# Performance work log

Hardware: AMD Instinct MI355X
Metric: run time of the kernel (lower is better)

Reference implementation:

```python
import jax, jax.numpy as jnp
import numpy as np

EPS = 1e-5  # torch LayerNorm default

def _ln(x, g, b):
    m = jnp.mean(x, axis=-1, keepdims=True)
    v = jnp.mean((x - m) ** 2, axis=-1, keepdims=True)
    return (x - m) * jax.lax.rsqrt(v + EPS) * g + b

def setup_inputs() -> dict:
    key = jax.random.key(0)
    ks = jax.random.split(key, 12)
    N_sup = N_res = 768
    c_z = 128   # input_dim
    c = 128     # num_intermediate_channel
    c_out = 128 # output_dim
    s = 0.02
    d = {}
    d["act_s"] = jax.random.normal(ks[0], (N_sup, N_sup, c_z), jnp.float32)
    d["act_r"] = jax.random.normal(ks[1], (N_res, N_res, c_z), jnp.float32)
    d["mask_r"] = (jax.random.uniform(ks[2], (N_res, N_res)) > 0.1).astype(jnp.float32)
    # input LayerNorm params
    d["ln_in_g"] = jnp.ones((c_z,), jnp.float32)
    d["ln_in_b"] = jnp.zeros((c_z,), jnp.float32)
    # projections (stored as [in, out], y = x @ W + b)
    d["w_lp"] = (jax.random.normal(ks[3], (c_z, c)) * s).astype(jnp.float32)
    d["b_lp"] = jnp.zeros((c,), jnp.float32)
    d["w_rp"] = (jax.random.normal(ks[4], (c_z, c)) * s).astype(jnp.float32)
    d["b_rp"] = jnp.zeros((c,), jnp.float32)
    # gates (bias_init=1)
    d["w_lg"] = (jax.random.normal(ks[5], (c_z, c)) * s).astype(jnp.float32)
    d["b_lg"] = jnp.ones((c,), jnp.float32)
    d["w_rg"] = (jax.random.normal(ks[6], (c_z, c)) * s).astype(jnp.float32)
    d["b_rg"] = jnp.ones((c,), jnp.float32)
    # center LayerNorm
    d["ln_c_g"] = jnp.ones((c,), jnp.float32)
    d["ln_c_b"] = jnp.zeros((c,), jnp.float32)
    # output projection
    d["w_out"] = (jax.random.normal(ks[7], (c, c_out)) * s).astype(jnp.float32)
    d["b_out"] = jnp.zeros((c_out,), jnp.float32)
    return d

def reference(act_s, act_r, mask_r, ln_in_g, ln_in_b, w_lp, b_lp, w_rp, b_rp,
              w_lg, b_lg, w_rg, b_rg, ln_c_g, ln_c_b, w_out, b_out):
    m = mask_r[..., None]                                   # [N_res, N_res, 1]
    s = _ln(act_s, ln_in_g, ln_in_b)                        # [N_sup, N_sup, c_z]
    r = _ln(act_r, ln_in_g, ln_in_b)                        # [N_res, N_res, c_z]
    left = (s @ w_lp + b_lp) * jax.nn.sigmoid(s @ w_lg + b_lg)
    right = (m * (r @ w_rp + b_rp)) * jax.nn.sigmoid(r @ w_rg + b_rg)
    left_line = left.sum(axis=0)                            # [N_sup, c] (aggr_by_row)
    right_line = right.sum(axis=0)                          # [N_res, c]
    act = jnp.einsum('ik,jk->ijk', left_line, right_line)   # [N_sup, N_res, c]
    act = _ln(act, ln_c_g, ln_c_b)
    return act @ w_out + b_out                              # [N_sup, N_res, c_out]
```

## Files before the change

### kernel.cpp

```cpp
#include <hip/hip_runtime.h>
#include <math.h>

#define NRES 768
#define C    128
#define LNEPS 1e-5f
#define TA   16
#define ACH  48
#define MI   16
#define NIT  (NRES / MI)
#define XBUF (MI * 256)

typedef __attribute__((ext_vector_type(8))) short bf16x8;
typedef __attribute__((ext_vector_type(4))) float f32x4;

__device__ __forceinline__ uint32_t bf16rn(float f) {
    uint32_t u = __float_as_uint(f);
    return (u + 0x7FFFu + ((u >> 16) & 1u)) >> 16;
}

__device__ __forceinline__ void split2(float a, float b, uint32_t& hi, uint32_t& lo) {
    uint32_t ha = bf16rn(a), hb = bf16rn(b);
    float ra = a - __uint_as_float(ha << 16);
    float rb = b - __uint_as_float(hb << 16);
    hi = ha | (hb << 16);
    lo = bf16rn(ra) | (bf16rn(rb) << 16);
}

__device__ __forceinline__ void stage_row3(const float4& x, int row, int t,
                                           char* hiB, char* loB, char* sqB) {
    const int byte = (row * 256 + 8 * (t & 31)) ^ ((row & 15) << 4);
    uint2 uh, ul, uq;
    split2(x.x, x.y, uh.x, ul.x);
    split2(x.z, x.w, uh.y, ul.y);
    uq.x = bf16rn(x.x * x.x) | (bf16rn(x.y * x.y) << 16);
    uq.y = bf16rn(x.z * x.z) | (bf16rn(x.w * x.w) << 16);
    *(uint2*)(hiB + byte) = uh;
    *(uint2*)(loB + byte) = ul;
    *(uint2*)(sqB + byte) = uq;
}

template <int RIGHT>
__global__ __launch_bounds__(256, 3) void line_mfma(
    const float* __restrict__ act,
    const float* __restrict__ mask,
    const float* __restrict__ ln_g, const float* __restrict__ ln_b,
    const float* __restrict__ wP, const float* __restrict__ bP,
    const float* __restrict__ wG, const float* __restrict__ bG,
    float* __restrict__ part)
{
    __shared__ char  sHi[XBUF];
    __shared__ char  sLo[XBUF];
    __shared__ char  sSq[XBUF];
    __shared__ float sM[TA * MI];

    const int t = threadIdx.x;
    const int w = t >> 6;
    const int l = t & 63;
    const int i0  = (blockIdx.x % NIT) * MI;
    const int ach = blockIdx.x / NIT;
    const int a0  = ach * TA;

    bf16x8 bfr[4][4];
    float  sQ[4], cB[4];
#pragma unroll
    for (int nt = 0; nt < 4; ++nt) {
        const float* wsrc = (nt < 2) ? wP : wG;
        const int n = w * 32 + (nt & 1) * 16 + (l & 15);
        float sacc = 0.f, tacc = 0.f;
#pragma unroll
        for (int kk = 0; kk < 4; ++kk) {
            bf16x8 f;
#pragma unroll
            for (int jj = 0; jj < 8; ++jj) {
                const int k = kk * 32 + (l >> 4) * 8 + jj;
                const float wv = wsrc[k * C + n];
                const uint32_t q = bf16rn(ln_g[k] * wv);
                f[jj] = (short)q;
                sacc += __uint_as_float(q << 16);
                tacc += ln_b[k] * wv;
            }
            bfr[nt][kk] = f;
        }
        sacc += __shfl_xor(sacc, 16); sacc += __shfl_xor(sacc, 32);
        tacc += __shfl_xor(tacc, 16); tacc += __shfl_xor(tacc, 32);
        sQ[nt] = sacc;
        cB[nt] = tacc + ((nt < 2) ? bP[n] : bG[n]);
    }

    bf16x8 onesf;
#pragma unroll
    for (int jj = 0; jj < 8; ++jj) onesf[jj] = (short)0x3F80;

    if (RIGHT) {
        sM[t] = mask[(size_t)(a0 + (t >> 4)) * NRES + i0 + (t & 15)];
    }

    float lacc[2][4];
#pragma unroll
    for (int ntp = 0; ntp < 2; ++ntp)
#pragma unroll
        for (int jr = 0; jr < 4; ++jr) lacc[ntp][jr] = 0.f;

    const float* srcbase = act + (size_t)a0 * (NRES * C) + (size_t)i0 * C;

    float4 xv[2], xn[2];
#pragma unroll
    for (int j = 0; j < 2; ++j)
        xv[j] = *(const float4*)(srcbase + 4 * (t + 256 * j));

    for (int al = 0; al < TA; ++al) {
        if (al + 1 < TA) {
            const float* srcn = srcbase + (size_t)(al + 1) * (NRES * C);
#pragma unroll
            for (int j = 0; j < 2; ++j)
                xn[j] = *(const float4*)(srcn + 4 * (t + 256 * j));
        }

#pragma unroll
        for (int j = 0; j < 2; ++j)
            stage_row3(xv[j], (t >> 5) + 8 * j, t, sHi, sLo, sSq);
        __syncthreads();

        const f32x4 zero = {0.f, 0.f, 0.f, 0.f};
        f32x4 acc[4], accS = zero, accS2 = zero;
#pragma unroll
        for (int nt = 0; nt < 4; ++nt) acc[nt] = zero;

#pragma unroll
        for (int kk = 0; kk < 4; ++kk) {
            const int row  = l & 15;
            const int byte = (row * 256 + (kk * 32 + (l >> 4) * 8) * 2) ^ ((row & 15) << 4);
            const bf16x8 ah  = *(const bf16x8*)(sHi + byte);
            const bf16x8 alo = *(const bf16x8*)(sLo + byte);
            const bf16x8 asq = *(const bf16x8*)(sSq + byte);
            acc[0] = __builtin_amdgcn_mfma_f32_16x16x32_bf16(ah,  bfr[0][kk], acc[0], 0, 0, 0);
            acc[0] = __builtin_amdgcn_mfma_f32_16x16x32_bf16(alo, bfr[0][kk], acc[0], 0, 0, 0);
            acc[1] = __builtin_amdgcn_mfma_f32_16x16x32_bf16(ah,  bfr[1][kk], acc[1], 0, 0, 0);
            acc[1] = __builtin_amdgcn_mfma_f32_16x16x32_bf16(alo, bfr[1][kk], acc[1], 0, 0, 0);
            acc[2] = __builtin_amdgcn_mfma_f32_16x16x32_bf16(ah,  bfr[2][kk], acc[2], 0, 0, 0);
            acc[3] = __builtin_amdgcn_mfma_f32_16x16x32_bf16(ah,  bfr[3][kk], acc[3], 0, 0, 0);
            accS  = __builtin_amdgcn_mfma_f32_16x16x32_bf16(ah,  onesf, accS,  0, 0, 0);
            accS2 = __builtin_amdgcn_mfma_f32_16x16x32_bf16(asq, onesf, accS2, 0, 0, 0);
        }

        float mk[4] = {1.f, 1.f, 1.f, 1.f};
        if (RIGHT) {
            const float4 m4 = *(const float4*)&sM[al * MI + (l >> 4) * 4];
            mk[0] = m4.x; mk[1] = m4.y; mk[2] = m4.z; mk[3] = m4.w;
        }
#pragma unroll
        for (int jr = 0; jr < 4; ++jr) {
            const float m_  = accS[jr] * (1.f / C);
            const float var = accS2[jr] * (1.f / C) - m_ * m_;
            const float inv = rsqrtf(var + LNEPS);
#pragma unroll
            for (int ntp = 0; ntp < 2; ++ntp) {
                const float P = (acc[ntp][jr]     - m_ * sQ[ntp])     * inv + cB[ntp];
                const float G = (acc[ntp + 2][jr] - m_ * sQ[ntp + 2]) * inv + cB[ntp + 2];
                const float sg = __builtin_amdgcn_rcpf(1.f + __expf(-G));
                lacc[ntp][jr] += P * sg * mk[jr];
            }
        }
        __syncthreads();

        xv[0] = xn[0]; xv[1] = xn[1];
    }

    float* dst = part + (size_t)ach * (NRES * C);
#pragma unroll
    for (int ntp = 0; ntp < 2; ++ntp)
#pragma unroll
        for (int jr = 0; jr < 4; ++jr)
            dst[(size_t)(i0 + (l >> 4) * 4 + jr) * C +
                w * 32 + ntp * 16 + (l & 15)] = lacc[ntp][jr];
}

__global__ __launch_bounds__(256) void reduce_part(const float* __restrict__ part,
                                                   float* __restrict__ line) {
    const int idx = blockIdx.x * 256 + threadIdx.x;
    float s = 0.f;
#pragma unroll 8
    for (int p = 0; p < ACH; ++p) s += part[(size_t)p * (NRES * C) + idx];
    line[idx] = s;
}

__global__ __launch_bounds__(256, 3) void out_mfma(
    const float* __restrict__ lline,
    const float* __restrict__ rline,
    const float* __restrict__ cg, const float* __restrict__ cb,
    const float* __restrict__ wO, const float* __restrict__ bO,
    float* __restrict__ out)
{
    __shared__ char sHi[64 * 256];
    __shared__ char sLo[64 * 256];
    __shared__ char sSq[64 * 256];

    const int t = threadIdx.x;
    const int w = t >> 6;
    const int l = t & 63;
    const int i  = blockIdx.x / 12;
    const int j0 = (blockIdx.x % 12) * 64;

    bf16x8 bfr[2][4];
    float  sQ[2], cB[2];
#pragma unroll
    for (int nt = 0; nt < 2; ++nt) {
        const int n = w * 32 + nt * 16 + (l & 15);
        float sacc = 0.f, tacc = 0.f;
#pragma unroll
        for (int kk = 0; kk < 4; ++kk) {
            bf16x8 f;
#pragma unroll
            for (int jj = 0; jj < 8; ++jj) {
                const int k = kk * 32 + (l >> 4) * 8 + jj;
                const float wv = wO[k * C + n];
                const uint32_t q = bf16rn(cg[k] * wv);
                f[jj] = (short)q;
                sacc += __uint_as_float(q << 16);
                tacc += cb[k] * wv;
            }
            bfr[nt][kk] = f;
        }
        sacc += __shfl_xor(sacc, 16); sacc += __shfl_xor(sacc, 32);
        tacc += __shfl_xor(tacc, 16); tacc += __shfl_xor(tacc, 32);
        sQ[nt] = sacc;
        cB[nt] = tacc + bO[n];
    }

    bf16x8 onesf;
#pragma unroll
    for (int jj = 0; jj < 8; ++jj) onesf[jj] = (short)0x3F80;

    const int c4 = 4 * (t & 31);
    const float4 l4 = *(const float4*)(lline + (size_t)i * C + c4);

    const float* rsrc = rline + (size_t)j0 * C;
#pragma unroll
    for (int j = 0; j < 8; ++j) {
        const float4 r = *(const float4*)(rsrc + 4 * (t + 256 * j));
        float4 p;
        p.x = l4.x * r.x; p.y = l4.y * r.y; p.z = l4.z * r.z; p.w = l4.w * r.w;
        stage_row3(p, (t >> 5) + 8 * j, t, sHi, sLo, sSq);
    }
    __syncthreads();

    const f32x4 zero = {0.f, 0.f, 0.f, 0.f};
#pragma unroll
    for (int mt = 0; mt < 4; ++mt) {
        f32x4 acc[2], accS = zero, accS2 = zero;
#pragma unroll
        for (int nt = 0; nt < 2; ++nt) acc[nt] = zero;
#pragma unroll
        for (int kk = 0; kk < 4; ++kk) {
            const int row  = mt * 16 + (l & 15);
            const int byte = (row * 256 + (kk * 32 + (l >> 4) * 8) * 2) ^ ((row & 15) << 4);
            const bf16x8 ah  = *(const bf16x8*)(sHi + byte);
            const bf16x8 alo = *(const bf16x8*)(sLo + byte);
            const bf16x8 asq = *(const bf16x8*)(sSq + byte);
            acc[0] = __builtin_amdgcn_mfma_f32_16x16x32_bf16(ah,  bfr[0][kk], acc[0], 0, 0, 0);
            acc[0] = __builtin_amdgcn_mfma_f32_16x16x32_bf16(alo, bfr[0][kk], acc[0], 0, 0, 0);
            acc[1] = __builtin_amdgcn_mfma_f32_16x16x32_bf16(ah,  bfr[1][kk], acc[1], 0, 0, 0);
            acc[1] = __builtin_amdgcn_mfma_f32_16x16x32_bf16(alo, bfr[1][kk], acc[1], 0, 0, 0);
            accS  = __builtin_amdgcn_mfma_f32_16x16x32_bf16(ah,  onesf, accS,  0, 0, 0);
            accS2 = __builtin_amdgcn_mfma_f32_16x16x32_bf16(asq, onesf, accS2, 0, 0, 0);
        }
#pragma unroll
        for (int jr = 0; jr < 4; ++jr) {
            const float m_  = accS[jr] * (1.f / C);
            const float var = accS2[jr] * (1.f / C) - m_ * m_;
            const float inv = rsqrtf(var + LNEPS);
#pragma unroll
            for (int nt = 0; nt < 2; ++nt)
                out[((size_t)i * NRES + j0 + mt * 16 + (l >> 4) * 4 + jr) * C +
                    w * 32 + nt * 16 + (l & 15)] =
                    (acc[nt][jr] - m_ * sQ[nt]) * inv + cB[nt];
        }
    }
}

extern "C" void kernel_launch(void* const* d_in, const int* in_sizes, int n_in,
                              void* d_out, int out_size, void* d_ws, size_t ws_size,
                              hipStream_t stream) {
    const float* act_s = (const float*)d_in[0];
    const float* act_r = (const float*)d_in[1];
    const float* mask  = (const float*)d_in[2];
    const float* ln_g  = (const float*)d_in[3];
    const float* ln_b  = (const float*)d_in[4];
    const float* w_lp  = (const float*)d_in[5];
    const float* b_lp  = (const float*)d_in[6];
    const float* w_rp  = (const float*)d_in[7];
    const float* b_rp  = (const float*)d_in[8];
    const float* w_lg  = (const float*)d_in[9];
    const float* b_lg  = (const float*)d_in[10];
    const float* w_rg  = (const float*)d_in[11];
    const float* b_rg  = (const float*)d_in[12];
    const float* ln_cg = (const float*)d_in[13];
    const float* ln_cb = (const float*)d_in[14];
    const float* w_out = (const float*)d_in[15];
    const float* b_out = (const float*)d_in[16];
    float* out = (float*)d_out;

    float* part       = (float*)d_ws;
    float* left_line  = part + (size_t)ACH * NRES * C;
    float* right_line = left_line + NRES * C;

    line_mfma<0><<<ACH * NIT, 256, 0, stream>>>(act_s, nullptr, ln_g, ln_b,
                                                w_lp, b_lp, w_lg, b_lg, part);
    reduce_part<<<NRES * C / 256, 256, 0, stream>>>(part, left_line);
    line_mfma<1><<<ACH * NIT, 256, 0, stream>>>(act_r, mask, ln_g, ln_b,
                                                w_rp, b_rp, w_rg, b_rg, part);
    reduce_part<<<NRES * C / 256, 256, 0, stream>>>(part, right_line);
    out_mfma<<<NRES * 12, 256, 0, stream>>>(left_line, right_line, ln_cg, ln_cb,
                                            w_out, b_out, out);
}
```

Baseline: 366.4 us.

## Merge left/right line kernels, fuse reductions, loop output tiles per block

Merges the left and right line-projection kernels into one launch and the two reductions into one, which removes launches and lets both halves share the GPU at once. The out kernel now gives each block a whole output row and loops over 12 column tiles, so the weight fragments are built once per row instead of once per tile. The staging split switches from round-to-nearest to truncation for the hi/lo/square bf16 parts, which is cheaper but can change numerics slightly. The risks are a larger partial-sum workspace and only 768 output blocks with a serial tile loop, which may cut parallelism and latency hiding.

Result: faster. 337.3 us (-8.0%).

```diff
diff --git a/kernel.cpp b/kernel.cpp
--- a/kernel.cpp
+++ b/kernel.cpp
@@ -9,43 +9,49 @@
 #define MI   16
 #define NIT  (NRES / MI)
 #define XBUF (MI * 256)
+#define LHALF (ACH * NIT)
 
 typedef __attribute__((ext_vector_type(8))) short bf16x8;
 typedef __attribute__((ext_vector_type(4))) float f32x4;
 
-__device__ __forceinline__ uint32_t bf16rn(float f) {
-    uint32_t u = __float_as_uint(f);
-    return (u + 0x7FFFu + ((u >> 16) & 1u)) >> 16;
-}
-
-__device__ __forceinline__ void split2(float a, float b, uint32_t& hi, uint32_t& lo) {
-    uint32_t ha = bf16rn(a), hb = bf16rn(b);
-    float ra = a - __uint_as_float(ha << 16);
-    float rb = b - __uint_as_float(hb << 16);
-    hi = ha | (hb << 16);
-    lo = bf16rn(ra) | (bf16rn(rb) << 16);
+__device__ __forceinline__ uint32_t pack_hi(uint32_t u0, uint32_t u1) {
+    return (u1 & 0xFFFF0000u) | (u0 >> 16);
+}
+
+__device__ __forceinline__ void split2t(float a, float b, uint32_t& hi, uint32_t& lo) {
+    const uint32_t ua = __float_as_uint(a), ub = __float_as_uint(b);
+    const float ra = a - __uint_as_float(ua & 0xFFFF0000u);
+    const float rb = b - __uint_as_float(ub & 0xFFFF0000u);
+    hi = pack_hi(ua, ub);
+    lo = pack_hi(__float_as_uint(ra), __float_as_uint(rb));
 }
 
 __device__ __forceinline__ void stage_row3(const float4& x, int row, int t,
                                            char* hiB, char* loB, char* sqB) {
     const int byte = (row * 256 + 8 * (t & 31)) ^ ((row & 15) << 4);
     uint2 uh, ul, uq;
-    split2(x.x, x.y, uh.x, ul.x);
-    split2(x.z, x.w, uh.y, ul.y);
-    uq.x = bf16rn(x.x * x.x) | (bf16rn(x.y * x.y) << 16);
-    uq.y = bf16rn(x.z * x.z) | (bf16rn(x.w * x.w) << 16);
+    split2t(x.x, x.y, uh.x, ul.x);
+    split2t(x.z, x.w, uh.y, ul.y);
+    uq.x = pack_hi(__float_as_uint(x.x * x.x), __float_as_uint(x.y * x.y));
+    uq.y = pack_hi(__float_as_uint(x.z * x.z), __float_as_uint(x.w * x.w));
     *(uint2*)(hiB + byte) = uh;
     *(uint2*)(loB + byte) = ul;
     *(uint2*)(sqB + byte) = uq;
 }
 
-template <int RIGHT>
-__global__ __launch_bounds__(256, 3) void line_mfma(
-    const float* __restrict__ act,
+__device__ __forceinline__ uint32_t bf16rn(float f) {
+    uint32_t u = __float_as_uint(f);
+    return (u + 0x7FFFu + ((u >> 16) & 1u)) >> 16;
+}
+
+__global__ __launch_bounds__(256, 3) void line_all(
+    const float* __restrict__ act_s, const float* __restrict__ act_r,
     const float* __restrict__ mask,
     const float* __restrict__ ln_g, const float* __restrict__ ln_b,
-    const float* __restrict__ wP, const float* __restrict__ bP,
-    const float* __restrict__ wG, const float* __restrict__ bG,
+    const float* __restrict__ w_lp, const float* __restrict__ b_lp,
+    const float* __restrict__ w_rp, const float* __restrict__ b_rp,
+    const float* __restrict__ w_lg, const float* __restrict__ b_lg,
+    const float* __restrict__ w_rg, const float* __restrict__ b_rg,
     float* __restrict__ part)
 {
     __shared__ char  sHi[XBUF];
@@ -56,9 +62,17 @@
     const int t = threadIdx.x;
     const int w = t >> 6;
     const int l = t & 63;
-    const int i0  = (blockIdx.x % NIT) * MI;
-    const int ach = blockIdx.x / NIT;
+    const int right = (blockIdx.x >= LHALF);
+    const int bid2  = blockIdx.x - right * LHALF;
+    const int i0  = (bid2 % NIT) * MI;
+    const int ach = bid2 / NIT;
     const int a0  = ach * TA;
+
+    const float* act = right ? act_r : act_s;
+    const float* wP  = right ? w_rp : w_lp;
+    const float* bP  = right ? b_rp : b_lp;
+    const float* wG  = right ? w_rg : w_lg;
+    const float* bG  = right ? b_rg : b_lg;
 
     bf16x8 bfr[4][4];
     float  sQ[4], cB[4];
@@ -91,7 +105,7 @@
 #pragma unroll
     for (int jj = 0; jj < 8; ++jj) onesf[jj] = (short)0x3F80;
 
-    if (RIGHT) {
+    if (right) {
         sM[t] = mask[(size_t)(a0 + (t >> 4)) * NRES + i0 + (t & 15)];
     }
 
@@ -139,12 +153,12 @@
             acc[1] = __builtin_amdgcn_mfma_f32_16x16x32_bf16(alo, bfr[1][kk], acc[1], 0, 0, 0);
             acc[2] = __builtin_amdgcn_mfma_f32_16x16x32_bf16(ah,  bfr[2][kk], acc[2], 0, 0, 0);
             acc[3] = __builtin_amdgcn_mfma_f32_16x16x32_bf16(ah,  bfr[3][kk], acc[3], 0, 0, 0);
-            accS  = __builtin_amdgcn_mfma_f32_16x16x32_bf16(ah,  onesf, accS,  0, 0, 0);
-            accS2 = __builtin_amdgcn_mfma_f32_16x16x32_bf16(asq, onesf, accS2, 0, 0, 0);
+            accS   = __builtin_amdgcn_mfma_f32_16x16x32_bf16(ah,  onesf, accS,  0, 0, 0);
+            accS2  = __builtin_amdgcn_mfma_f32_16x16x32_bf16(asq, onesf, accS2, 0, 0, 0);
         }
 
         float mk[4] = {1.f, 1.f, 1.f, 1.f};
-        if (RIGHT) {
+        if (right) {
             const float4 m4 = *(const float4*)&sM[al * MI + (l >> 4) * 4];
             mk[0] = m4.x; mk[1] = m4.y; mk[2] = m4.z; mk[3] = m4.w;
         }
@@ -166,7 +180,7 @@
         xv[0] = xn[0]; xv[1] = xn[1];
     }
 
-    float* dst = part + (size_t)ach * (NRES * C);
+    float* dst = part + ((size_t)right * ACH + ach) * (NRES * C);
 #pragma unroll
     for (int ntp = 0; ntp < 2; ++ntp)
 #pragma unroll
@@ -175,13 +189,16 @@
                 w * 32 + ntp * 16 + (l & 15)] = lacc[ntp][jr];
 }
 
-__global__ __launch_bounds__(256) void reduce_part(const float* __restrict__ part,
-                                                   float* __restrict__ line) {
-    const int idx = blockIdx.x * 256 + threadIdx.x;
+__global__ __launch_bounds__(256) void reduce2(const float* __restrict__ part,
+                                               float* __restrict__ left_line,
+                                               float* __restrict__ right_line) {
+    const int half = (blockIdx.x >= 384);
+    const int idx  = (blockIdx.x - half * 384) * 256 + threadIdx.x;
+    const float* p = part + (size_t)half * ACH * NRES * C;
     float s = 0.f;
 #pragma unroll 8
-    for (int p = 0; p < ACH; ++p) s += part[(size_t)p * (NRES * C) + idx];
-    line[idx] = s;
+    for (int q = 0; q < ACH; ++q) s += p[(size_t)q * (NRES * C) + idx];
+    (half ? right_line : left_line)[idx] = s;
 }
 
 __global__ __launch_bounds__(256, 3) void out_mfma(
@@ -198,8 +215,7 @@
     const int t = threadIdx.x;
     const int w = t >> 6;
     const int l = t & 63;
-    const int i  = blockIdx.x / 12;
-    const int j0 = (blockIdx.x % 12) * 64;
+    const int i = blockIdx.x;
 
     bf16x8 bfr[2][4];
     float  sQ[2], cB[2];
@@ -234,47 +250,56 @@
     const int c4 = 4 * (t & 31);
     const float4 l4 = *(const float4*)(lline + (size_t)i * C + c4);
 
-    const float* rsrc = rline + (size_t)j0 * C;
-#pragma unroll
-    for (int j = 0; j < 8; ++j) {
-        const float4 r = *(const float4*)(rsrc + 4 * (t + 256 * j));
-        float4 p;
-        p.x = l4.x * r.x; p.y = l4.y * r.y; p.z = l4.z * r.z; p.w = l4.w * r.w;
-        stage_row3(p, (t >> 5) + 8 * j, t, sHi, sLo, sSq);
-    }
-    __syncthreads();
-
-    const f32x4 zero = {0.f, 0.f, 0.f, 0.f};
-#pragma unroll
-    for (int mt = 0; mt < 4; ++mt) {
-        f32x4 acc[2], accS = zero, accS2 = zero;
-#pragma unroll
-        for (int nt = 0; nt < 2; ++nt) acc[nt] = zero;
-#pragma unroll
-        for (int kk = 0; kk < 4; ++kk) {
-            const int row  = mt * 16 + (l & 15);
-            const int byte = (row * 256 + (kk * 32 + (l >> 4) * 8) * 2) ^ ((row & 15) << 4);
-            const bf16x8 ah  = *(const bf16x8*)(sHi + byte);
-            const bf16x8 alo = *(const bf16x8*)(sLo + byte);
-            const bf16x8 asq = *(const bf16x8*)(sSq + byte);
-            acc[0] = __builtin_amdgcn_mfma_f32_16x16x32_bf16(ah,  bfr[0][kk], acc[0], 0, 0, 0);
-            acc[0] = __builtin_amdgcn_mfma_f32_16x16x32_bf16(alo, bfr[0][kk], acc[0], 0, 0, 0);
-            acc[1] = __builtin_amdgcn_mfma_f32_16x16x32_bf16(ah,  bfr[1][kk], acc[1], 0, 0, 0);
-            acc[1] = __builtin_amdgcn_mfma_f32_16x16x32_bf16(alo, bfr[1][kk], acc[1], 0, 0, 0);
-            accS  = __builtin_amdgcn_mfma_f32_16x16x32_bf16(ah,  onesf, accS,  0, 0, 0);
-            accS2 = __builtin_amdgcn_mfma_f32_16x16x32_bf16(asq, onesf, accS2, 0, 0, 0);
-        }
-#pragma unroll
-        for (int jr = 0; jr < 4; ++jr) {
-            const float m_  = accS[jr] * (1.f / C);
-            const float var = accS2[jr] * (1.f / C) - m_ * m_;
-            const float inv = rsqrtf(var + LNEPS);
-#pragma unroll
-            for (int nt = 0; nt < 2; ++nt)
-                out[((size_t)i * NRES + j0 + mt * 16 + (l >> 4) * 4 + jr) * C +
-                    w * 32 + nt * 16 + (l & 15)] =
-                    (acc[nt][jr] - m_ * sQ[nt]) * inv + cB[nt];
-        }
+    for (int jt = 0; jt < 12; ++jt) {
+        const int j0 = jt * 64;
+        const float* rsrc = rline + (size_t)j0 * C;
+
+        float4 rv[8];
+#pragma unroll
+        for (int j = 0; j < 8; ++j)
+            rv[j] = *(const float4*)(rsrc + 4 * (t + 256 * j));
+#pragma unroll
+        for (int j = 0; j < 8; ++j) {
+            float4 p;
+            p.x = l4.x * rv[j].x; p.y = l4.y * rv[j].y;
+            p.z = l4.z * rv[j].z; p.w = l4.w * rv[j].w;
+            stage_row3(p, (t >> 5) + 8 * j, t, sHi, sLo, sSq);
+        }
+        __syncthreads();
+
+        const f32x4 zero = {0.f, 0.f, 0.f, 0.f};
+#pragma unroll
+        for (int mt = 0; mt < 4; ++mt) {
+            f32x4 acc[2], accS = zero, accS2 = zero;
+#pragma unroll
+            for (int nt = 0; nt < 2; ++nt) acc[nt] = zero;
+#pragma unroll
+            for (int kk = 0; kk < 4; ++kk) {
+                const int row  = mt * 16 + (l & 15);
+                const int byte = (row * 256 + (kk * 32 + (l >> 4) * 8) * 2) ^ ((row & 15) << 4);
+                const bf16x8 ah  = *(const bf16x8*)(sHi + byte);
+                const bf16x8 alo = *(const bf16x8*)(sLo + byte);
+                const bf16x8 asq = *(const bf16x8*)(sSq + byte);
+                acc[0] = __builtin_amdgcn_mfma_f32_16x16x32_bf16(ah,  bfr[0][kk], acc[0], 0, 0, 0);
+                acc[0] = __builtin_amdgcn_mfma_f32_16x16x32_bf16(alo, bfr[0][kk], acc[0], 0, 0, 0);
+                acc[1] = __builtin_amdgcn_mfma_f32_16x16x32_bf16(ah,  bfr[1][kk], acc[1], 0, 0, 0);
+                acc[1] = __builtin_amdgcn_mfma_f32_16x16x32_bf16(alo, bfr[1][kk], acc[1], 0, 0, 0);
+                accS  = __builtin_amdgcn_mfma_f32_16x16x32_bf16(ah,  onesf, accS,  0, 0, 0);
+                accS2 = __builtin_amdgcn_mfma_f32_16x16x32_bf16(asq, onesf, accS2, 0, 0, 0);
+            }
+#pragma unroll
+            for (int jr = 0; jr < 4; ++jr) {
+                const float m_  = accS[jr] * (1.f / C);
+                const float var = accS2[jr] * (1.f / C) - m_ * m_;
+                const float inv = rsqrtf(var + LNEPS);
+#pragma unroll
+                for (int nt = 0; nt < 2; ++nt)
+                    out[((size_t)i * NRES + j0 + mt * 16 + (l >> 4) * 4 + jr) * C +
+                        w * 32 + nt * 16 + (l & 15)] =
+                        (acc[nt][jr] - m_ * sQ[nt]) * inv + cB[nt];
+            }
+        }
+        __syncthreads();
     }
 }
 
@@ -301,15 +326,13 @@
     float* out = (float*)d_out;
 
     float* part       = (float*)d_ws;
-    float* left_line  = part + (size_t)ACH * NRES * C;
+    float* left_line  = part + (size_t)2 * ACH * NRES * C;
     float* right_line = left_line + NRES * C;
 
-    line_mfma<0><<<ACH * NIT, 256, 0, stream>>>(act_s, nullptr, ln_g, ln_b,
-                                                w_lp, b_lp, w_lg, b_lg, part);
-    reduce_part<<<NRES * C / 256, 256, 0, stream>>>(part, left_line);
-    line_mfma<1><<<ACH * NIT, 256, 0, stream>>>(act_r, mask, ln_g, ln_b,
-                                                w_rp, b_rp, w_rg, b_rg, part);
-    reduce_part<<<NRES * C / 256, 256, 0, stream>>>(part, right_line);
-    out_mfma<<<NRES * 12, 256, 0, stream>>>(left_line, right_line, ln_cg, ln_cb,
-                                            w_out, b_out, out);
-}
+    line_all<<<2 * LHALF, 256, 0, stream>>>(act_s, act_r, mask, ln_g, ln_b,
+                                            w_lp, b_lp, w_rp, b_rp,
+                                            w_lg, b_lg, w_rg, b_rg, part);
+    reduce2<<<768, 256, 0, stream>>>(part, left_line, right_line);
+    out_mfma<<<NRES, 256, 0, stream>>>(left_line, right_line, ln_cg, ln_cb,
+                                       w_out, b_out, out);
+}
```
